# Kernel optimization log

Hardware: AMD Instinct MI355X
Metric: run time of the kernel (lower is better)

The kernel has to match this reference:

```python
import jax, jax.numpy as jnp
import numpy as np

N_SEGMENT = 8
NUM_HEADS = 4
KERNEL = 5
PAD_L = 4  # causal left padding (kernel_size - 1)


def setup_inputs() -> dict:
    key = jax.random.key(0)
    k1, k2 = jax.random.split(key)
    x = jax.random.normal(k1, (128, 512, 14, 14), dtype=jnp.float32)
    W_weight = jax.random.normal(k2, (NUM_HEADS * KERNEL, 512), dtype=jnp.float32) * 0.02
    return {"x": x, "W_weight": W_weight}


def reference(x, W_weight):
    nt, c, h, w = x.shape
    T = N_SEGMENT
    n = nt // T
    B = n * h * w
    H, K, R = NUM_HEADS, KERNEL, c // NUM_HEADS

    # (nt, c, h, w) -> (n, T, c, h, w) -> permute(1,0,3,4,2) -> (T, B, c)
    xt = x.reshape(n, T, c, h, w).transpose(1, 0, 3, 4, 2).reshape(T, B, c)

    # per-position dynamic kernels: Linear(c -> H*K), softmax over kernel taps
    w_logits = jnp.einsum('tbc,oc->tbo', xt, W_weight).reshape(T, B, H, K)
    weights = jax.nn.softmax(w_logits, axis=-1)  # (T, B, H, K)

    # causal banded unfold: window[t, ..., k] = x[t + k - PAD_L], zeros outside
    xpad = jnp.pad(xt, ((PAD_L, 0), (0, 0), (0, 0)))  # (T+4, B, c)
    windows = jnp.stack([xpad[k:k + T] for k in range(K)], axis=-1)  # (T, B, c, K)
    win = windows.reshape(T, B, H, R, K)

    out = jnp.einsum('tbhrk,tbhk->tbhr', win, weights).reshape(T, B, c)

    # (T, n, h, w, c) -> permute(1,0,4,2,3) -> (nt, c, h, w)
    out = out.reshape(T, n, h, w, c).transpose(1, 0, 4, 2, 3).reshape(nt, c, h, w)
    return out
```

## Files before the change

kernel.cpp:

```cpp
#include <hip/hip_runtime.h>

#define T 8
#define C 512
#define HW 196
#define NSEG 16
#define NT (NSEG * T)
#define B_TOT (NSEG * HW)
#define NH 4
#define KK 5
#define NO 20
#define S_SPLIT 8
#define CCH (C / S_SPLIT)

__global__ __launch_bounds__(256) void k_logits(const float* __restrict__ x,
                                                const float* __restrict__ W,
                                                float* __restrict__ pl) {
    const int idx = blockIdx.x * 256 + threadIdx.x;
    const int nt  = idx / HW;
    const int hw  = idx - nt * HW;
    const int s   = blockIdx.y;
    const int cbase = s * CCH;

    const float* xp = x + ((size_t)nt * C + cbase) * HW + hw;

    float acc[NO];
#pragma unroll
    for (int o = 0; o < NO; ++o) acc[o] = 0.f;

    float xv[8], xn[8];
#pragma unroll
    for (int u = 0; u < 8; ++u) xv[u] = xp[u * HW];

#pragma unroll
    for (int c0 = 0; c0 < CCH; c0 += 8) {
        if (c0 + 8 < CCH) {
#pragma unroll
            for (int u = 0; u < 8; ++u) xn[u] = xp[(c0 + 8 + u) * HW];
        }
        const float* wr = W + cbase + c0;
#pragma unroll
        for (int o = 0; o < NO; ++o) {
#pragma unroll
            for (int u = 0; u < 8; ++u)
                acc[o] = fmaf(xv[u], wr[o * C + u], acc[o]);
        }
#pragma unroll
        for (int u = 0; u < 8; ++u) xv[u] = xn[u];
    }

    float* pp = pl + ((size_t)(s * NT + nt) * NO) * HW + hw;
#pragma unroll
    for (int o = 0; o < NO; ++o) pp[o * HW] = acc[o];
}

__global__ __launch_bounds__(256) void k_softmax(const float* __restrict__ pl,
                                                 float* __restrict__ wgt) {
    const int b = blockIdx.x * 256 + threadIdx.x;
    const int t = blockIdx.y;
    const int h = blockIdx.z;
    if (b >= B_TOT) return;
    const int n  = b / HW;
    const int hw = b - n * HW;
    const int nt = n * T + t;

    float lg[KK];
#pragma unroll
    for (int k = 0; k < KK; ++k) {
        float sm = 0.f;
#pragma unroll
        for (int s = 0; s < S_SPLIT; ++s)
            sm += pl[((size_t)(s * NT + nt) * NO + h * KK + k) * HW + hw];
        lg[k] = sm;
    }

    float m = lg[0];
#pragma unroll
    for (int k = 1; k < KK; ++k) m = fmaxf(m, lg[k]);
    float e[KK];
    float sum = 0.f;
#pragma unroll
    for (int k = 0; k < KK; ++k) {
        e[k] = __expf(lg[k] - m);
        sum += e[k];
    }
    const float r = 1.f / sum;
#pragma unroll
    for (int k = 0; k < KK; ++k)
        wgt[((size_t)((t * NH + h) * KK + k)) * B_TOT + b] = e[k] * r;
}

__global__ __launch_bounds__(256) void k_conv(const float* __restrict__ x,
                                              const float* __restrict__ wgt,
                                              float* __restrict__ out) {
    const int idx = blockIdx.x * 256 + threadIdx.x;
    const int hw  = idx % HW;
    const int t1  = idx / HW;
    const int c   = t1 % C;
    const int n   = t1 / C;
    const int h   = c >> 7;
    const int b   = n * HW + hw;

    float w[T][KK];
#pragma unroll
    for (int t = 0; t < T; ++t)
#pragma unroll
        for (int k = 0; k < KK; ++k)
            w[t][k] = wgt[((size_t)((t * NH + h) * KK + k)) * B_TOT + b];

    const size_t base = ((size_t)(n * T) * C + c) * HW + hw;
    float xv[T];
#pragma unroll
    for (int t = 0; t < T; ++t) xv[t] = x[base + (size_t)t * C * HW];

#pragma unroll
    for (int t = 0; t < T; ++t) {
        float acc = 0.f;
#pragma unroll
        for (int k = 0; k < KK; ++k) {
            const int j = t + k - 4;
            if (j >= 0) acc = fmaf(w[t][k], xv[j], acc);
        }
        out[base + (size_t)t * C * HW] = acc;
    }
}

extern "C" void kernel_launch(void* const* d_in, const int* in_sizes, int n_in,
                              void* d_out, int out_size, void* d_ws, size_t ws_size,
                              hipStream_t stream) {
    const float* x = (const float*)d_in[0];
    const float* W = (const float*)d_in[1];
    float* out = (float*)d_out;

    float* pl  = (float*)d_ws;
    float* wgt = pl + (size_t)S_SPLIT * NT * NO * HW;

    k_logits<<<dim3(25088 / 256, S_SPLIT), 256, 0, stream>>>(x, W, pl);
    k_softmax<<<dim3((B_TOT + 255) / 256, T, NH), 256, 0, stream>>>(pl, wgt);
    k_conv<<<dim3((NSEG * C * HW) / 256), 256, 0, stream>>>(x, wgt, out);
}
```

Measured before the change: 125.3 us.

## Fuse logits and softmax into one kernel with LDS split-K reduction

Merges the logits kernel and the softmax kernel into a single kernel. Each block handles 32 columns, and its 8 warps each take a channel slice. Partial logits are reduced through shared memory instead of a global workspace, which removes the write and re-read of 8 split partial buffers and one launch. In exchange, each block reads only 32 columns with 32-lane contiguous accesses, and only half the threads do the softmax step.

New measurement: 142.8 us. 1.14x slower.

```diff
diff --git a/kernel.cpp b/kernel.cpp
--- a/kernel.cpp
+++ b/kernel.cpp
@@ -5,21 +5,27 @@
 #define HW 196
 #define NSEG 16
 #define NT (NSEG * T)
+#define NCOL (NT * HW)
 #define B_TOT (NSEG * HW)
 #define NH 4
 #define KK 5
 #define NO 20
 #define S_SPLIT 8
 #define CCH (C / S_SPLIT)
+#define COLS 32
 
-__global__ __launch_bounds__(256) void k_logits(const float* __restrict__ x,
-                                                const float* __restrict__ W,
-                                                float* __restrict__ pl) {
-    const int idx = blockIdx.x * 256 + threadIdx.x;
-    const int nt  = idx / HW;
-    const int hw  = idx - nt * HW;
-    const int s   = blockIdx.y;
-    const int cbase = s * CCH;
+__global__ __launch_bounds__(256) void k_weights(const float* __restrict__ x,
+                                                 const float* __restrict__ W,
+                                                 float* __restrict__ wgt) {
+    __shared__ float plds[S_SPLIT][NO][COLS];
+
+    const int tid  = threadIdx.x;
+    const int sch  = tid >> 5;
+    const int j    = tid & 31;
+    const int idx  = blockIdx.x * COLS + j;
+    const int nt   = idx / HW;
+    const int hw   = idx - nt * HW;
+    const int cbase = sch * CCH;
 
     const float* xp = x + ((size_t)nt * C + cbase) * HW + hw;
 
@@ -48,45 +54,45 @@
         for (int u = 0; u < 8; ++u) xv[u] = xn[u];
     }
 
-    float* pp = pl + ((size_t)(s * NT + nt) * NO) * HW + hw;
 #pragma unroll
-    for (int o = 0; o < NO; ++o) pp[o * HW] = acc[o];
-}
+    for (int o = 0; o < NO; ++o) plds[sch][o][j] = acc[o];
+    __syncthreads();
 
-__global__ __launch_bounds__(256) void k_softmax(const float* __restrict__ pl,
-                                                 float* __restrict__ wgt) {
-    const int b = blockIdx.x * 256 + threadIdx.x;
-    const int t = blockIdx.y;
-    const int h = blockIdx.z;
-    if (b >= B_TOT) return;
-    const int n  = b / HW;
-    const int hw = b - n * HW;
-    const int nt = n * T + t;
+    if (tid < COLS * NH) {
+        const int col  = tid & 31;
+        const int h    = tid >> 5;
+        const int idx2 = blockIdx.x * COLS + col;
+        const int nt2  = idx2 / HW;
+        const int hw2  = idx2 - nt2 * HW;
+        const int t    = nt2 & (T - 1);
+        const int n    = nt2 / T;
+        const int b    = n * HW + hw2;
 
-    float lg[KK];
+        float lg[KK];
 #pragma unroll
-    for (int k = 0; k < KK; ++k) {
-        float sm = 0.f;
+        for (int k = 0; k < KK; ++k) {
+            float sm = 0.f;
 #pragma unroll
-        for (int s = 0; s < S_SPLIT; ++s)
-            sm += pl[((size_t)(s * NT + nt) * NO + h * KK + k) * HW + hw];
-        lg[k] = sm;
+            for (int s2 = 0; s2 < S_SPLIT; ++s2)
+                sm += plds[s2][h * KK + k][col];
+            lg[k] = sm;
+        }
+
+        float m = lg[0];
+#pragma unroll
+        for (int k = 1; k < KK; ++k) m = fmaxf(m, lg[k]);
+        float e[KK];
+        float sum = 0.f;
+#pragma unroll
+        for (int k = 0; k < KK; ++k) {
+            e[k] = __expf(lg[k] - m);
+            sum += e[k];
+        }
+        const float r = 1.f / sum;
+#pragma unroll
+        for (int k = 0; k < KK; ++k)
+            wgt[((size_t)((t * NH + h) * KK + k)) * B_TOT + b] = e[k] * r;
     }
-
-    float m = lg[0];
-#pragma unroll
-    for (int k = 1; k < KK; ++k) m = fmaxf(m, lg[k]);
-    float e[KK];
-    float sum = 0.f;
-#pragma unroll
-    for (int k = 0; k < KK; ++k) {
-        e[k] = __expf(lg[k] - m);
-        sum += e[k];
-    }
-    const float r = 1.f / sum;
-#pragma unroll
-    for (int k = 0; k < KK; ++k)
-        wgt[((size_t)((t * NH + h) * KK + k)) * B_TOT + b] = e[k] * r;
 }
 
 __global__ __launch_bounds__(256) void k_conv(const float* __restrict__ x,
@@ -131,10 +137,8 @@
     const float* W = (const float*)d_in[1];
     float* out = (float*)d_out;
 
-    float* pl  = (float*)d_ws;
-    float* wgt = pl + (size_t)S_SPLIT * NT * NO * HW;
+    float* wgt = (float*)d_ws;
 
-    k_logits<<<dim3(25088 / 256, S_SPLIT), 256, 0, stream>>>(x, W, pl);
-    k_softmax<<<dim3((B_TOT + 255) / 256, T, NH), 256, 0, stream>>>(pl, wgt);
+    k_weights<<<dim3(NCOL / COLS), 256, 0, stream>>>(x, W, wgt);
     k_conv<<<dim3((NSEG * C * HW) / 256), 256, 0, stream>>>(x, wgt, out);
 }
```
